# Optimization experiments

Measured on AMD Instinct MI355X. Metric: run time of the kernel, lower is better.

## Reference

```python
import jax, jax.numpy as jnp
import numpy as np

B = 512      # batch
T = 128      # decoder horizon -> T-1 = 127 steps
DNH = 128    # decoder_num_hidden
ENC = 2 * DNH   # encoder_num_hidden (required by attn concat: 3*ENC == 6*DNH)
H = 2 * DNH     # LSTM hidden size


def setup_inputs() -> dict:
    key = jax.random.key(0)
    ks = jax.random.split(key, 10)
    def w(k, shape, scale=0.05):
        return jax.random.normal(k, shape, jnp.float32) * scale
    return {
        "X_encoded": jax.random.normal(ks[0], (B, T - 1, ENC), jnp.float32),
        "y_prev":    jax.random.normal(ks[1], (B, T - 1), jnp.float32),
        # attn_layer: Linear(6*DNH -> DNH) then Linear(DNH -> 1)
        "W_attn1": w(ks[2], (DNH, 6 * DNH)), "b_attn1": jnp.zeros((DNH,), jnp.float32),
        "W_attn2": w(ks[3], (1, DNH)),       "b_attn2": jnp.zeros((1,), jnp.float32),
        # fc: Linear(2*DNH+1 -> 1)
        "W_fc": w(ks[4], (1, 2 * DNH + 1)),  "b_fc": jnp.zeros((1,), jnp.float32),
        # single-layer LSTM, input_size=1, hidden=H, PyTorch gate order (i,f,g,o)
        "W_ih": w(ks[5], (4 * H, 1)), "W_hh": w(ks[6], (4 * H, H)),
        "b_ih": jnp.zeros((4 * H,), jnp.float32), "b_hh": jnp.zeros((4 * H,), jnp.float32),
        # fc_final: Linear(4*DNH -> 1)
        "W_final": w(ks[7], (1, 4 * DNH)), "b_final": jnp.zeros((1,), jnp.float32),
    }


def reference(X_encoded, y_prev, W_attn1, b_attn1, W_attn2, b_attn2,
              W_fc, b_fc, W_ih, W_hh, b_ih, b_hh, W_final, b_final):
    Bz, Tm1, E = X_encoded.shape
    Hh = W_hh.shape[1]
    d0 = jnp.zeros((Bz, Hh), X_encoded.dtype)
    c0 = jnp.zeros((Bz, Hh), X_encoded.dtype)

    def step(carry, y_t):
        d, c = carry                                   # (B, H) each
        state = jnp.concatenate([d, c], axis=-1)[:, None, :]        # (B,1,2H)
        x = jnp.concatenate(
            [jnp.broadcast_to(state, (Bz, Tm1, 2 * Hh)), X_encoded], axis=-1)  # (B,T-1,6*DNH)
        a = x @ W_attn1.T + b_attn1                    # (B,T-1,DNH)
        score = (a @ W_attn2.T + b_attn2)[..., 0]      # (B,T-1)
        beta = jax.nn.softmax(score, axis=1)
        context = jnp.einsum('bt,bte->be', beta, X_encoded)          # (B,E)
        y = jnp.concatenate([context, y_t[:, None]], axis=-1)        # (B,E+1)
        y_tilde = y @ W_fc.T + b_fc                    # (B,1)
        gates = y_tilde @ W_ih.T + b_ih + d @ W_hh.T + b_hh          # (B,4H)
        i, f, g, o = jnp.split(gates, 4, axis=-1)
        i, f, o = jax.nn.sigmoid(i), jax.nn.sigmoid(f), jax.nn.sigmoid(o)
        g = jnp.tanh(g)
        c_new = f * c + i * g
        d_new = o * jnp.tanh(c_new)
        return (d_new, c_new), context

    (dT, _), contexts = jax.lax.scan(step, (d0, c0), y_prev.T)
    y_pred = jnp.concatenate([dT, contexts[-1]], axis=-1) @ W_final.T + b_final  # (B,1)
    return y_pred
```

## Files before the change

kernel.cpp:

```cpp
#include <hip/hip_runtime.h>
#include <stdint.h>

typedef __attribute__((ext_vector_type(8))) short short8;
typedef __attribute__((ext_vector_type(8))) unsigned short ushort8_t;
typedef __attribute__((ext_vector_type(4))) float floatx4;

#define T1 127
#define ENC 256
#define HD 256

#define WHI_OFF   0u
#define WLO_OFF   524288u
#define D0_OFF    1048576u
#define D1_OFF    1572864u
#define WEFF_OFF  2097152u
#define YT_OFF    2099200u
#define CTX_OFF   2361344u
#define DT_OFF    2885632u

__device__ __forceinline__ void split_bf16(float x, unsigned& hi, unsigned& lo) {
    unsigned u = __float_as_uint(x);
    hi = u >> 16;
    float hf = __uint_as_float(hi << 16);
    float r = x - hf;
    unsigned ur = __float_as_uint(r);
    lo = (ur + 0x7fffu + ((ur >> 16) & 1u)) >> 16;
}

__device__ __forceinline__ float sigm_f(float x) { return 1.f / (1.f + __expf(-x)); }
__device__ __forceinline__ float tanh_f(float x) {
    x = fminf(9.f, fmaxf(-9.f, x));
    float e = __expf(2.f * x);
    return (e - 1.f) / (e + 1.f);
}

__device__ __forceinline__ void load64_ag(const unsigned long long* p,
                                          uint4& a, uint4& b, uint4& c, uint4& d) {
    asm volatile("global_load_dwordx4 %0, %4, off sc0 sc1\n\t"
                 "global_load_dwordx4 %1, %4, off offset:16 sc0 sc1\n\t"
                 "global_load_dwordx4 %2, %4, off offset:32 sc0 sc1\n\t"
                 "global_load_dwordx4 %3, %4, off offset:48 sc0 sc1\n\t"
                 "s_waitcnt vmcnt(0)"
                 : "=v"(a), "=v"(b), "=v"(c), "=v"(d)
                 : "v"((unsigned long long)p)
                 : "memory");
}

__global__ __launch_bounds__(256) void k_prep(const float* __restrict__ W1,
                                              const float* __restrict__ W2,
                                              const float* __restrict__ W_hh,
                                              char* __restrict__ ws) {
    const int tid = threadIdx.x, bid = blockIdx.x;
    ushort* Whi = (ushort*)(ws + WHI_OFF);
    ushort* Wlo = (ushort*)(ws + WLO_OFF);
    {
        const int i4 = bid * 256 + tid;
        float4 v = ((const float4*)W_hh)[i4];
        float vv[4] = {v.x, v.y, v.z, v.w};
        unsigned h[4], l[4];
        #pragma unroll
        for (int j = 0; j < 4; ++j) split_bf16(vv[j], h[j], l[j]);
        *(ushort4*)(Whi + i4 * 4) = make_ushort4((ushort)h[0], (ushort)h[1], (ushort)h[2], (ushort)h[3]);
        *(ushort4*)(Wlo + i4 * 4) = make_ushort4((ushort)l[0], (ushort)l[1], (ushort)l[2], (ushort)l[3]);
    }
    {
        const int idx = bid * 256 + tid;
        if (idx < 32768) ((uint4*)(ws + D0_OFF))[idx] = make_uint4(0, 0, 0, 0);
    }
    if (bid == 0) {
        float acc = 0.f;
        for (int j = 0; j < 128; ++j)
            acc = fmaf(W2[j], W1[j * 768 + 512 + tid], acc);
        ((float*)(ws + WEFF_OFF))[tid] = acc;
    }
}

__global__ __launch_bounds__(256) void k_attn(const float* __restrict__ X,
                                              const float* __restrict__ y_prev,
                                              const float* __restrict__ W_fc,
                                              const float* __restrict__ b_fc,
                                              char* __restrict__ ws) {
    __shared__ float s_lds[128];
    __shared__ float beta[128];
    __shared__ float red[256];
    const int b = blockIdx.x, tid = threadIdx.x;
    const int w = tid >> 6, lane = tid & 63;
    const float* Xb = X + (size_t)b * T1 * ENC;
    const float* weff = (const float*)(ws + WEFF_OFF);
    const float4 w4 = ((const float4*)weff)[lane];
    for (int i = 0; i < 32; ++i) {
        int t = w * 32 + i;
        if (t >= T1) break;
        float4 x4 = ((const float4*)(Xb + t * ENC))[lane];
        float a = x4.x * w4.x + x4.y * w4.y + x4.z * w4.z + x4.w * w4.w;
        for (int m = 32; m >= 1; m >>= 1) a += __shfl_xor(a, m, 64);
        if (lane == 0) s_lds[t] = a;
    }
    __syncthreads();
    if (w == 0) {
        float v0 = s_lds[lane];
        float v1 = (lane + 64 < T1) ? s_lds[lane + 64] : -1e30f;
        float mx = fmaxf(v0, v1);
        for (int m = 32; m >= 1; m >>= 1) mx = fmaxf(mx, __shfl_xor(mx, m, 64));
        float e0 = __expf(v0 - mx);
        float e1 = (lane + 64 < T1) ? __expf(v1 - mx) : 0.f;
        float s = e0 + e1;
        for (int m = 32; m >= 1; m >>= 1) s += __shfl_xor(s, m, 64);
        float inv = 1.f / s;
        beta[lane] = e0 * inv;
        if (lane + 64 < T1) beta[lane + 64] = e1 * inv;
    }
    __syncthreads();
    float acc = 0.f;
    for (int t = 0; t < T1; ++t) acc = fmaf(beta[t], Xb[t * ENC + tid], acc);
    ((float*)(ws + CTX_OFF))[b * ENC + tid] = acc;
    red[tid] = acc * W_fc[tid];
    __syncthreads();
    for (int s = 128; s >= 1; s >>= 1) { if (tid < s) red[tid] += red[tid + s]; __syncthreads(); }
    const float u = red[0] + b_fc[0];
    const float wy = W_fc[256];
    if (tid < T1)
        ((float*)(ws + YT_OFF))[b * 128 + tid] = u + wy * y_prev[b * T1 + tid];
}

__global__ __launch_bounds__(256, 1) void k_lstm(const float* __restrict__ W_ih,
                                                 const float* __restrict__ b_ih,
                                                 const float* __restrict__ b_hh,
                                                 char* __restrict__ ws) {
    __shared__ __align__(16) ushort ldh[16 * 264];
    __shared__ __align__(16) ushort ldl[16 * 264];
    __shared__ float gbuf[16 * 132];

    const int tid = threadIdx.x, bid = blockIdx.x;
    const int gi = bid >> 3, hj = bid & 7;
    const int w = tid >> 6, lane = tid & 63;
    const int n16 = lane & 15, q = lane >> 4;

    const ushort* Whi = (const ushort*)(ws + WHI_OFF);
    const ushort* Wlo = (const ushort*)(ws + WLO_OFF);
    unsigned long long* Dbuf0 = (unsigned long long*)(ws + D0_OFF);
    unsigned long long* Dbuf1 = (unsigned long long*)(ws + D1_OFF);
    const float* yt = (const float*)(ws + YT_OFF);
    float* dT = (float*)(ws + DT_OFF);

    short8 bfh[2][8], bfl[2][8];
    #pragma unroll
    for (int j = 0; j < 2; ++j) {
        const int r = (2 * w + j) * 16 + n16;
        const int hloc = r >> 2, g = r & 3;
        const int R = g * 256 + hj * 32 + hloc;
        #pragma unroll
        for (int kt = 0; kt < 8; ++kt) {
            bfh[j][kt] = *(const short8*)(Whi + R * 256 + kt * 32 + q * 8);
            bfl[j][kt] = *(const short8*)(Wlo + R * 256 + kt * 32 + q * 8);
        }
    }

    const int b_loc = tid & 15, hpair = tid >> 4;
    const int hloc0 = hpair * 2;
    const int bg = gi * 16 + b_loc;
    float wihr[2][4], bihr[2][4];
    #pragma unroll
    for (int jj = 0; jj < 2; ++jj)
        #pragma unroll
        for (int g = 0; g < 4; ++g) {
            const int row = g * HD + hj * 32 + hloc0 + jj;
            wihr[jj][g] = W_ih[row];
            bihr[jj][g] = b_ih[row] + b_hh[row];
        }
    float cc0 = 0.f, cc1 = 0.f;

    const int pb = tid >> 4, hp8 = tid & 15;
    const bool own = ((hp8 >> 1) == hj);
    const size_t pbase = (size_t)(gi * 16 + pb) * 128 + hp8 * 8;

    {
        ushort8_t z = {0, 0, 0, 0, 0, 0, 0, 0};
        *(ushort8_t*)(ldh + pb * 264 + hp8 * 16)     = z;
        *(ushort8_t*)(ldh + pb * 264 + hp8 * 16 + 8) = z;
        *(ushort8_t*)(ldl + pb * 264 + hp8 * 16)     = z;
        *(ushort8_t*)(ldl + pb * 264 + hp8 * 16 + 8) = z;
    }

    for (int t = 1; t <= T1; ++t) {
        const float ytv = yt[bg * 128 + (t - 1)];
        if (!own) {
            unsigned long long* Dsrc = ((t - 1) & 1) ? Dbuf1 : Dbuf0;
            const unsigned e = (unsigned)(t - 1) & 3u;
            unsigned lo[8], hi[8];
            for (int round = 0; ; ++round) {
                uint4 A, B, C, D;
                load64_ag(&Dsrc[pbase], A, B, C, D);
                lo[0] = A.x; hi[0] = A.y; lo[1] = A.z; hi[1] = A.w;
                lo[2] = B.x; hi[2] = B.y; lo[3] = B.z; hi[3] = B.w;
                lo[4] = C.x; hi[4] = C.y; lo[5] = C.z; hi[5] = C.w;
                lo[6] = D.x; hi[6] = D.y; lo[7] = D.z; hi[7] = D.w;
                bool ok = true;
                #pragma unroll
                for (int i = 0; i < 8; ++i) {
                    unsigned ep = (lo[i] & 1u) | ((hi[i] & 1u) << 1);
                    ok &= (ep == e);
                }
                if (ok) break;
                if (round >= 16) __builtin_amdgcn_s_sleep(1);
            }
            ushort hv[16], lv[16];
            #pragma unroll
            for (int i = 0; i < 8; ++i) {
                hv[2 * i]     = (ushort)(lo[i] >> 16);
                hv[2 * i + 1] = (ushort)(hi[i] >> 16);
                lv[2 * i]     = (ushort)(lo[i] & 0xFFFEu);
                lv[2 * i + 1] = (ushort)(hi[i] & 0xFFFEu);
            }
            ushort8_t H0, L0, H1, L1;
            #pragma unroll
            for (int i = 0; i < 8; ++i) { H0[i] = hv[i]; L0[i] = lv[i]; H1[i] = hv[8 + i]; L1[i] = lv[8 + i]; }
            *(ushort8_t*)(ldh + pb * 264 + hp8 * 16)     = H0;
            *(ushort8_t*)(ldh + pb * 264 + hp8 * 16 + 8) = H1;
            *(ushort8_t*)(ldl + pb * 264 + hp8 * 16)     = L0;
            *(ushort8_t*)(ldl + pb * 264 + hp8 * 16 + 8) = L1;
        }
        __syncthreads();
        floatx4 acc0 = {0.f, 0.f, 0.f, 0.f}, acc1 = {0.f, 0.f, 0.f, 0.f};
        #pragma unroll
        for (int kt = 0; kt < 8; ++kt) {
            short8 ah = *(const short8*)(ldh + n16 * 264 + kt * 32 + q * 8);
            short8 al = *(const short8*)(ldl + n16 * 264 + kt * 32 + q * 8);
            acc0 = __builtin_amdgcn_mfma_f32_16x16x32_bf16(ah, bfh[0][kt], acc0, 0, 0, 0);
            acc0 = __builtin_amdgcn_mfma_f32_16x16x32_bf16(al, bfh[0][kt], acc0, 0, 0, 0);
            acc0 = __builtin_amdgcn_mfma_f32_16x16x32_bf16(ah, bfl[0][kt], acc0, 0, 0, 0);
            acc1 = __builtin_amdgcn_mfma_f32_16x16x32_bf16(ah, bfh[1][kt], acc1, 0, 0, 0);
            acc1 = __builtin_amdgcn_mfma_f32_16x16x32_bf16(al, bfh[1][kt], acc1, 0, 0, 0);
            acc1 = __builtin_amdgcn_mfma_f32_16x16x32_bf16(ah, bfl[1][kt], acc1, 0, 0, 0);
        }
        #pragma unroll
        for (int reg = 0; reg < 4; ++reg) {
            gbuf[(q * 4 + reg) * 132 + (2 * w) * 16 + n16]     = acc0[reg];
            gbuf[(q * 4 + reg) * 132 + (2 * w + 1) * 16 + n16] = acc1[reg];
        }
        __syncthreads();
        float dnew[2];
        #pragma unroll
        for (int jj = 0; jj < 2; ++jj) {
            const int base = b_loc * 132 + (hloc0 + jj) * 4;
            float pi = gbuf[base + 0] + ytv * wihr[jj][0] + bihr[jj][0];
            float pf = gbuf[base + 1] + ytv * wihr[jj][1] + bihr[jj][1];
            float pg = gbuf[base + 2] + ytv * wihr[jj][2] + bihr[jj][2];
            float po = gbuf[base + 3] + ytv * wihr[jj][3] + bihr[jj][3];
            float ig = sigm_f(pi), fg = sigm_f(pf), og = sigm_f(po);
            float gg = tanh_f(pg);
            float& c = jj ? cc1 : cc0;
            c = fg * c + ig * gg;
            dnew[jj] = og * tanh_f(c);
        }
        if (t < T1) {
            const unsigned e = (unsigned)t & 3u;
            unsigned h0, l0, h1, l1;
            split_bf16(dnew[0], h0, l0);
            split_bf16(dnew[1], h1, l1);
            l0 = (l0 & 0xFFFEu) | (e & 1u);
            l1 = (l1 & 0xFFFEu) | ((e >> 1) & 1u);
            unsigned long long wv = ((unsigned long long)h1 << 48) |
                                    ((unsigned long long)l1 << 32) |
                                    ((unsigned long long)h0 << 16) |
                                    (unsigned long long)l0;
            unsigned long long* Ddst = (t & 1) ? Dbuf1 : Dbuf0;
            __hip_atomic_store(&Ddst[(size_t)bg * 128 + hj * 16 + hpair], wv,
                               __ATOMIC_RELAXED, __HIP_MEMORY_SCOPE_AGENT);
            *(ushort2*)(ldh + b_loc * 264 + hj * 32 + hloc0) =
                make_ushort2((ushort)h0, (ushort)h1);
            *(ushort2*)(ldl + b_loc * 264 + hj * 32 + hloc0) =
                make_ushort2((ushort)(l0 & 0xFFFEu), (ushort)(l1 & 0xFFFEu));
        } else {
            *(float2*)(dT + bg * 256 + hj * 32 + hloc0) = make_float2(dnew[0], dnew[1]);
        }
    }
}

__global__ __launch_bounds__(256) void k_final(const float* __restrict__ W_final,
                                               const float* __restrict__ b_final,
                                               float* __restrict__ out,
                                               char* __restrict__ ws) {
    __shared__ float red[256];
    const int b = blockIdx.x, tid = threadIdx.x;
    const float* dT = (const float*)(ws + DT_OFF);
    const float* ctx = (const float*)(ws + CTX_OFF);
    float v = W_final[tid] * dT[b * 256 + tid] + W_final[256 + tid] * ctx[b * 256 + tid];
    red[tid] = v;
    __syncthreads();
    for (int s = 128; s >= 1; s >>= 1) { if (tid < s) red[tid] += red[tid + s]; __syncthreads(); }
    if (tid == 0) out[b] = red[0] + b_final[0];
}

extern "C" void kernel_launch(void* const* d_in, const int* in_sizes, int n_in,
                              void* d_out, int out_size, void* d_ws, size_t ws_size,
                              hipStream_t stream) {
    const float* X      = (const float*)d_in[0];
    const float* y_prev = (const float*)d_in[1];
    const float* W1     = (const float*)d_in[2];
    const float* W2     = (const float*)d_in[4];
    const float* W_fc   = (const float*)d_in[6];
    const float* b_fc   = (const float*)d_in[7];
    const float* W_ih   = (const float*)d_in[8];
    const float* W_hh   = (const float*)d_in[9];
    const float* b_ih   = (const float*)d_in[10];
    const float* b_hh   = (const float*)d_in[11];
    const float* W_fin  = (const float*)d_in[12];
    const float* b_fin  = (const float*)d_in[13];
    char* ws = (char*)d_ws;

    hipLaunchKernelGGL(k_prep,  dim3(256), dim3(256), 0, stream, W1, W2, W_hh, ws);
    hipLaunchKernelGGL(k_attn,  dim3(512), dim3(256), 0, stream, X, y_prev, W_fc, b_fc, ws);
    hipLaunchKernelGGL(k_lstm,  dim3(256), dim3(256), 0, stream, W_ih, b_ih, b_hh, ws);
    hipLaunchKernelGGL(k_final, dim3(512), dim3(256), 0, stream, W_fin, b_fin, (float*)d_out, ws);
}
```

Before: 550.4 us.

## Fuse attention and weight split into LSTM kernel, drop context materialization

Removes the separate attention kernel and instead computes per-timestep projections of X onto the score, fc and final-layer weights inside the LSTM kernel prologue. Softmax weights then reduce these projections directly, so the full context vector is never stored. The bf16 hi/lo split of W_hh now happens on the fly when loading register fragments instead of in the prep kernel. This trades a kernel launch and intermediate traffic for redundant X reads across the 8 blocks sharing a batch group and a longer serial prologue per block.

```diff
diff --git a/kernel.cpp b/kernel.cpp
--- a/kernel.cpp
+++ b/kernel.cpp
@@ -9,13 +9,10 @@
 #define ENC 256
 #define HD 256
 
-#define WHI_OFF   0u
-#define WLO_OFF   524288u
 #define D0_OFF    1048576u
 #define D1_OFF    1572864u
 #define WEFF_OFF  2097152u
-#define YT_OFF    2099200u
-#define CTX_OFF   2361344u
+#define CF_OFF    2361344u
 #define DT_OFF    2885632u
 
 __device__ __forceinline__ void split_bf16(float x, unsigned& hi, unsigned& lo) {
@@ -48,21 +45,8 @@
 
 __global__ __launch_bounds__(256) void k_prep(const float* __restrict__ W1,
                                               const float* __restrict__ W2,
-                                              const float* __restrict__ W_hh,
                                               char* __restrict__ ws) {
     const int tid = threadIdx.x, bid = blockIdx.x;
-    ushort* Whi = (ushort*)(ws + WHI_OFF);
-    ushort* Wlo = (ushort*)(ws + WLO_OFF);
-    {
-        const int i4 = bid * 256 + tid;
-        float4 v = ((const float4*)W_hh)[i4];
-        float vv[4] = {v.x, v.y, v.z, v.w};
-        unsigned h[4], l[4];
-        #pragma unroll
-        for (int j = 0; j < 4; ++j) split_bf16(vv[j], h[j], l[j]);
-        *(ushort4*)(Whi + i4 * 4) = make_ushort4((ushort)h[0], (ushort)h[1], (ushort)h[2], (ushort)h[3]);
-        *(ushort4*)(Wlo + i4 * 4) = make_ushort4((ushort)l[0], (ushort)l[1], (ushort)l[2], (ushort)l[3]);
-    }
     {
         const int idx = bid * 256 + tid;
         if (idx < 32768) ((uint4*)(ws + D0_OFF))[idx] = make_uint4(0, 0, 0, 0);
@@ -75,73 +59,88 @@
     }
 }
 
-__global__ __launch_bounds__(256) void k_attn(const float* __restrict__ X,
-                                              const float* __restrict__ y_prev,
-                                              const float* __restrict__ W_fc,
-                                              const float* __restrict__ b_fc,
-                                              char* __restrict__ ws) {
-    __shared__ float s_lds[128];
-    __shared__ float beta[128];
-    __shared__ float red[256];
-    const int b = blockIdx.x, tid = threadIdx.x;
-    const int w = tid >> 6, lane = tid & 63;
-    const float* Xb = X + (size_t)b * T1 * ENC;
-    const float* weff = (const float*)(ws + WEFF_OFF);
-    const float4 w4 = ((const float4*)weff)[lane];
-    for (int i = 0; i < 32; ++i) {
-        int t = w * 32 + i;
-        if (t >= T1) break;
-        float4 x4 = ((const float4*)(Xb + t * ENC))[lane];
-        float a = x4.x * w4.x + x4.y * w4.y + x4.z * w4.z + x4.w * w4.w;
-        for (int m = 32; m >= 1; m >>= 1) a += __shfl_xor(a, m, 64);
-        if (lane == 0) s_lds[t] = a;
-    }
-    __syncthreads();
-    if (w == 0) {
-        float v0 = s_lds[lane];
-        float v1 = (lane + 64 < T1) ? s_lds[lane + 64] : -1e30f;
-        float mx = fmaxf(v0, v1);
-        for (int m = 32; m >= 1; m >>= 1) mx = fmaxf(mx, __shfl_xor(mx, m, 64));
-        float e0 = __expf(v0 - mx);
-        float e1 = (lane + 64 < T1) ? __expf(v1 - mx) : 0.f;
-        float s = e0 + e1;
-        for (int m = 32; m >= 1; m >>= 1) s += __shfl_xor(s, m, 64);
-        float inv = 1.f / s;
-        beta[lane] = e0 * inv;
-        if (lane + 64 < T1) beta[lane + 64] = e1 * inv;
-    }
-    __syncthreads();
-    float acc = 0.f;
-    for (int t = 0; t < T1; ++t) acc = fmaf(beta[t], Xb[t * ENC + tid], acc);
-    ((float*)(ws + CTX_OFF))[b * ENC + tid] = acc;
-    red[tid] = acc * W_fc[tid];
-    __syncthreads();
-    for (int s = 128; s >= 1; s >>= 1) { if (tid < s) red[tid] += red[tid + s]; __syncthreads(); }
-    const float u = red[0] + b_fc[0];
-    const float wy = W_fc[256];
-    if (tid < T1)
-        ((float*)(ws + YT_OFF))[b * 128 + tid] = u + wy * y_prev[b * T1 + tid];
-}
-
 __global__ __launch_bounds__(256, 1) void k_lstm(const float* __restrict__ W_ih,
                                                  const float* __restrict__ b_ih,
                                                  const float* __restrict__ b_hh,
+                                                 const float* __restrict__ W_hh,
+                                                 const float* __restrict__ X,
+                                                 const float* __restrict__ y_prev,
+                                                 const float* __restrict__ W_fc,
+                                                 const float* __restrict__ b_fc,
+                                                 const float* __restrict__ W_final,
                                                  char* __restrict__ ws) {
     __shared__ __align__(16) ushort ldh[16 * 264];
     __shared__ __align__(16) ushort ldl[16 * 264];
     __shared__ float gbuf[16 * 132];
+    __shared__ float s_sc[16 * 128];
+    __shared__ float s_xw[16 * 128];
+    __shared__ float s_xf[16 * 128];
+    __shared__ float s_u[16];
 
     const int tid = threadIdx.x, bid = blockIdx.x;
     const int gi = bid >> 3, hj = bid & 7;
     const int w = tid >> 6, lane = tid & 63;
     const int n16 = lane & 15, q = lane >> 4;
 
-    const ushort* Whi = (const ushort*)(ws + WHI_OFF);
-    const ushort* Wlo = (const ushort*)(ws + WLO_OFF);
     unsigned long long* Dbuf0 = (unsigned long long*)(ws + D0_OFF);
     unsigned long long* Dbuf1 = (unsigned long long*)(ws + D1_OFF);
-    const float* yt = (const float*)(ws + YT_OFF);
     float* dT = (float*)(ws + DT_OFF);
+    float* cf = (float*)(ws + CF_OFF);
+
+    {
+        const float* weff = (const float*)(ws + WEFF_OFF);
+        const float4 we4 = ((const float4*)weff)[lane];
+        const float4 wc4 = ((const float4*)W_fc)[lane];
+        const float4 wf4 = ((const float4*)(W_final + 256))[lane];
+        for (int bb = 0; bb < 16; ++bb) {
+            const float* Xb = X + (size_t)(gi * 16 + bb) * T1 * ENC;
+            #pragma unroll 4
+            for (int ti = 0; ti < 32; ++ti) {
+                const int t = w * 32 + ti;
+                if (t < T1) {
+                    float4 x4 = ((const float4*)(Xb + t * ENC))[lane];
+                    float as = x4.x * we4.x + x4.y * we4.y + x4.z * we4.z + x4.w * we4.w;
+                    float aw = x4.x * wc4.x + x4.y * wc4.y + x4.z * wc4.z + x4.w * wc4.w;
+                    float af = x4.x * wf4.x + x4.y * wf4.y + x4.z * wf4.z + x4.w * wf4.w;
+                    for (int m = 32; m >= 1; m >>= 1) {
+                        as += __shfl_xor(as, m, 64);
+                        aw += __shfl_xor(aw, m, 64);
+                        af += __shfl_xor(af, m, 64);
+                    }
+                    if (lane == 0) {
+                        s_sc[bb * 128 + t] = as;
+                        s_xw[bb * 128 + t] = aw;
+                        s_xf[bb * 128 + t] = af;
+                    }
+                }
+            }
+        }
+        __syncthreads();
+        for (int ii = 0; ii < 4; ++ii) {
+            const int bb = w + ii * 4;
+            const bool ok1 = (lane + 64 < T1);
+            float v0 = s_sc[bb * 128 + lane];
+            float v1 = ok1 ? s_sc[bb * 128 + lane + 64] : -1e30f;
+            float mx = fmaxf(v0, v1);
+            for (int m = 32; m >= 1; m >>= 1) mx = fmaxf(mx, __shfl_xor(mx, m, 64));
+            float e0 = __expf(v0 - mx);
+            float e1 = ok1 ? __expf(v1 - mx) : 0.f;
+            float s  = e0 + e1;
+            float uw = e0 * s_xw[bb * 128 + lane] + (ok1 ? e1 * s_xw[bb * 128 + lane + 64] : 0.f);
+            float uf = e0 * s_xf[bb * 128 + lane] + (ok1 ? e1 * s_xf[bb * 128 + lane + 64] : 0.f);
+            for (int m = 32; m >= 1; m >>= 1) {
+                s  += __shfl_xor(s, m, 64);
+                uw += __shfl_xor(uw, m, 64);
+                uf += __shfl_xor(uf, m, 64);
+            }
+            if (lane == 0) {
+                const float inv = 1.f / s;
+                s_u[bb] = uw * inv + b_fc[0];
+                if (hj == 0) cf[gi * 16 + bb] = uf * inv;
+            }
+        }
+        __syncthreads();
+    }
 
     short8 bfh[2][8], bfl[2][8];
     #pragma unroll
@@ -151,8 +150,18 @@
         const int R = g * 256 + hj * 32 + hloc;
         #pragma unroll
         for (int kt = 0; kt < 8; ++kt) {
-            bfh[j][kt] = *(const short8*)(Whi + R * 256 + kt * 32 + q * 8);
-            bfl[j][kt] = *(const short8*)(Wlo + R * 256 + kt * 32 + q * 8);
+            const float* src = W_hh + R * 256 + kt * 32 + q * 8;
+            float4 f0 = ((const float4*)src)[0];
+            float4 f1 = ((const float4*)src)[1];
+            float vv[8] = {f0.x, f0.y, f0.z, f0.w, f1.x, f1.y, f1.z, f1.w};
+            unsigned h[8], l[8];
+            #pragma unroll
+            for (int i = 0; i < 8; ++i) split_bf16(vv[i], h[i], l[i]);
+            short8 sh, sl;
+            #pragma unroll
+            for (int i = 0; i < 8; ++i) { sh[i] = (short)h[i]; sl[i] = (short)l[i]; }
+            bfh[j][kt] = sh;
+            bfl[j][kt] = sl;
         }
     }
 
@@ -169,6 +178,9 @@
             bihr[jj][g] = b_ih[row] + b_hh[row];
         }
     float cc0 = 0.f, cc1 = 0.f;
+    const float u_reg = s_u[b_loc];
+    const float wy = W_fc[256];
+    const float* ypb = y_prev + (size_t)bg * T1;
 
     const int pb = tid >> 4, hp8 = tid & 15;
     const bool own = ((hp8 >> 1) == hj);
@@ -183,7 +195,7 @@
     }
 
     for (int t = 1; t <= T1; ++t) {
-        const float ytv = yt[bg * 128 + (t - 1)];
+        const float ytv = u_reg + wy * ypb[t - 1];
         if (!own) {
             unsigned long long* Dsrc = ((t - 1) & 1) ? Dbuf1 : Dbuf0;
             const unsigned e = (unsigned)(t - 1) & 3u;
@@ -284,12 +296,11 @@
     __shared__ float red[256];
     const int b = blockIdx.x, tid = threadIdx.x;
     const float* dT = (const float*)(ws + DT_OFF);
-    const float* ctx = (const float*)(ws + CTX_OFF);
-    float v = W_final[tid] * dT[b * 256 + tid] + W_final[256 + tid] * ctx[b * 256 + tid];
-    red[tid] = v;
+    const float* cf = (const float*)(ws + CF_OFF);
+    red[tid] = W_final[tid] * dT[b * 256 + tid];
     __syncthreads();
     for (int s = 128; s >= 1; s >>= 1) { if (tid < s) red[tid] += red[tid + s]; __syncthreads(); }
-    if (tid == 0) out[b] = red[0] + b_final[0];
+    if (tid == 0) out[b] = red[0] + cf[b] + b_final[0];
 }
 
 extern "C" void kernel_launch(void* const* d_in, const int* in_sizes, int n_in,
@@ -309,8 +320,8 @@
     const float* b_fin  = (const float*)d_in[13];
     char* ws = (char*)d_ws;
 
-    hipLaunchKernelGGL(k_prep,  dim3(256), dim3(256), 0, stream, W1, W2, W_hh, ws);
-    hipLaunchKernelGGL(k_attn,  dim3(512), dim3(256), 0, stream, X, y_prev, W_fc, b_fc, ws);
-    hipLaunchKernelGGL(k_lstm,  dim3(256), dim3(256), 0, stream, W_ih, b_ih, b_hh, ws);
+    hipLaunchKernelGGL(k_prep,  dim3(128), dim3(256), 0, stream, W1, W2, ws);
+    hipLaunchKernelGGL(k_lstm,  dim3(256), dim3(256), 0, stream,
+                       W_ih, b_ih, b_hh, W_hh, X, y_prev, W_fc, b_fc, W_fin, ws);
     hipLaunchKernelGGL(k_final, dim3(512), dim3(256), 0, stream, W_fin, b_fin, (float*)d_out, ws);
 }
```

New measurement: 848.6 us. 1.54x slower.
